# Kernel optimization log

Hardware: AMD Instinct MI355X
Metric: run time of the kernel (lower is better)

The kernel has to match this reference:

```python
import jax, jax.numpy as jnp
import numpy as np

HEADS = 8
NBLK = 4  # N: 4x4 spatial blocks
DIM = 96
EPS_NORM = 1e-12  # torch F.normalize eps


def _blockify(t, head, n):
    # 'b (head c) (h1 hh) (w1 ww) -> b head c (h1 w1) (hh ww)'
    b, C, H, W = t.shape
    c, hh, ww = C // head, H // n, W // n
    t = t.reshape(b, head, c, n, hh, n, ww)
    return t.transpose(0, 1, 2, 3, 5, 4, 6).reshape(b, head, c, n * n, hh * ww)


def _unblockify(t, n, hh, ww):
    # inverse of _blockify
    b, head, c, _, _ = t.shape
    t = t.reshape(b, head, c, n, n, hh, ww).transpose(0, 1, 2, 3, 5, 4, 6)
    return t.reshape(b, head * c, n * hh, n * ww)


def _l2norm(t):
    return t / jnp.maximum(jnp.linalg.norm(t, axis=-1, keepdims=True), EPS_NORM)


def setup_inputs():
    key = jax.random.key(0)
    ks = jax.random.split(key, 5)
    b, dim, H, W = 4, DIM, 256, 256
    x = jax.random.normal(ks[0], (b, dim, H, W), jnp.float32)
    mask = jax.random.uniform(ks[1], (b, dim, H, W), jnp.float32)
    w_qkv = jax.random.normal(ks[2], (3 * dim, dim, 1, 1), jnp.float32) / np.sqrt(dim)
    w_dw = jax.random.normal(ks[3], (3 * dim, 1, 3, 3), jnp.float32) / 3.0
    w_proj = jax.random.normal(ks[4], (dim, dim, 1, 1), jnp.float32) / np.sqrt(dim)
    temp_x = jnp.ones((HEADS, 1, 1, 1), jnp.float32)
    temp_m = jnp.ones((HEADS, 1, 1, 1), jnp.float32)
    return {"x": x, "mask": mask, "w_qkv": w_qkv, "w_dw": w_dw,
            "w_proj": w_proj, "temp_x": temp_x, "temp_m": temp_m}


def reference(x, mask, w_qkv, w_dw, w_proj, temp_x, temp_m):
    # H, W chosen divisible by 4, so the reflect-pad in the original is a no-op.
    dn = ('NCHW', 'OIHW', 'NCHW')
    qkv = jax.lax.conv_general_dilated(x, w_qkv, (1, 1), 'VALID', dimension_numbers=dn)
    qkv = jax.lax.conv_general_dilated(qkv, w_dw, (1, 1), ((1, 1), (1, 1)),
                                       feature_group_count=qkv.shape[1],
                                       dimension_numbers=dn)
    q, k, v = jnp.split(qkv, 3, axis=1)
    q = _l2norm(_blockify(q, HEADS, NBLK))
    k = _l2norm(_blockify(k, HEADS, NBLK))
    v = _blockify(v, HEADS, NBLK)

    # channel-block attention: [b,head,c,16,16]; temp broadcasts over (b, c, 16, 16)
    attn_x = jax.nn.softmax(jnp.einsum('bhcns,bhcms->bhcnm', q, k) * temp_x, axis=-1)

    # mask-derived attention (MaskMap): q==k==blockified mask
    qm = _blockify(mask, HEADS, NBLK)
    attn_m = jnp.einsum('bhcns,bhcms->bhcnm', qm, qm) * temp_m
    attn_m = jax.nn.softmax(_l2norm(attn_m), axis=-1)

    attn = jax.nn.softmax(attn_x + attn_m, axis=-1)
    out = jnp.einsum('bhcnm,bhcms->bhcns', attn, v)

    hh, ww = x.shape[2] // NBLK, x.shape[3] // NBLK
    out = _unblockify(out, NBLK, hh, ww)
    out = jax.lax.conv_general_dilated(out, w_proj, (1, 1), 'VALID', dimension_numbers=dn)
    return out
```

## Files before the change

kernel.cpp:

```cpp
#include <hip/hip_runtime.h>
#include <math.h>

#define HPIX 256
#define WPIX 256
#define NPIX (HPIX * WPIX)
#define DIM 96
#define QKVC 288
#define NHEAD 8
#define CPH 12
#define EPSN 1e-12f
#define PSTRIDE 544

typedef __attribute__((ext_vector_type(8))) short bf16x8;
typedef __attribute__((ext_vector_type(4))) float f32x4;

__device__ __forceinline__ unsigned short f2bf(float f) {
  unsigned u = __float_as_uint(f);
  u += 0x7FFF + ((u >> 16) & 1);
  return (unsigned short)(u >> 16);
}
__device__ __forceinline__ float bf2f(unsigned short h) {
  return __uint_as_float((unsigned)h << 16);
}

__global__ __launch_bounds__(256) void k_wprep(
    const float* __restrict__ wq, const float* __restrict__ wp,
    unsigned short* __restrict__ wqbf, unsigned short* __restrict__ wpbf) {
  int i = blockIdx.x * 256 + threadIdx.x;
  if (i < QKVC * DIM) wqbf[i] = f2bf(wq[i]);
  if (i < DIM * DIM)  wpbf[i] = f2bf(wp[i]);
}

template<int OC, int OCB, typename InT, typename OutT>
__global__ __launch_bounds__(256, 3) void k_gemm1x1(
    const InT* __restrict__ xin, const unsigned short* __restrict__ wbf,
    OutT* __restrict__ out) {
  __shared__ __align__(16) unsigned short xT[128 * 128];
  __shared__ __align__(16) unsigned short wlds[OCB * 104];
  int t = threadIdx.x;
  int p0 = blockIdx.x * 128;
  int oc0 = blockIdx.y * OCB;
  const InT* xb = xin + (size_t)blockIdx.z * DIM * NPIX;

  for (int i = t; i < OCB * 12; i += 256) {
    int row = i / 12, seg = i % 12;
    bf16x8 w8 = *(const bf16x8*)(wbf + (size_t)(oc0 + row) * DIM + seg * 8);
    *(bf16x8*)&wlds[row * 104 + seg * 8] = w8;
  }
  if (t < 192) {
    int kg = t >> 4;
    int f4c = t & 15;
    #pragma unroll
    for (int rep = 0; rep < 2; ++rep) {
      int f4 = f4c + rep * 16;
      float vals[8][4];
      #pragma unroll
      for (int i = 0; i < 8; ++i) {
        if constexpr (sizeof(InT) == 2) {
          ushort4 v = *(const ushort4*)(xb + (size_t)(kg * 8 + i) * NPIX + p0 + f4 * 4);
          ((ushort*)vals[i])[0] = v.x; ((ushort*)vals[i])[1] = v.y;
          ((ushort*)vals[i])[2] = v.z; ((ushort*)vals[i])[3] = v.w;
        } else {
          float4 v = *(const float4*)(xb + (size_t)(kg * 8 + i) * NPIX + p0 + f4 * 4);
          vals[i][0] = v.x; vals[i][1] = v.y; vals[i][2] = v.z; vals[i][3] = v.w;
        }
      }
      #pragma unroll
      for (int c = 0; c < 4; ++c) {
        int px = f4 * 4 + c;
        int u = kg ^ ((px & 7) ^ ((px >> 3) & 7));
        bf16x8 hv;
        #pragma unroll
        for (int i = 0; i < 8; ++i) {
          if constexpr (sizeof(InT) == 2) hv[i] = (short)((ushort*)vals[i])[c];
          else                            hv[i] = (short)f2bf(vals[i][c]);
        }
        *(bf16x8*)&xT[px * 128 + u * 8] = hv;
      }
    }
  }
  __syncthreads();

  int lane = t & 63, wv = t >> 6;
  int r16 = lane & 15, kg8 = lane >> 4;

  bf16x8 bfr[3][2];
  #pragma unroll
  for (int nj = 0; nj < 2; ++nj) {
    int px = wv * 32 + nj * 16 + r16;
    int swz = (px & 7) ^ ((px >> 3) & 7);
    #pragma unroll
    for (int ks = 0; ks < 3; ++ks) {
      int u = (ks * 4 + kg8) ^ swz;
      bfr[ks][nj] = *(const bf16x8*)&xT[px * 128 + u * 8];
    }
  }

  f32x4 acc[OCB / 16][2];
  #pragma unroll
  for (int mi = 0; mi < OCB / 16; ++mi)
    #pragma unroll
    for (int nj = 0; nj < 2; ++nj) acc[mi][nj] = (f32x4){0.f, 0.f, 0.f, 0.f};

  #pragma unroll
  for (int mi = 0; mi < OCB / 16; ++mi) {
    #pragma unroll
    for (int ks = 0; ks < 3; ++ks) {
      bf16x8 a = *(const bf16x8*)&wlds[(mi * 16 + r16) * 104 + ks * 32 + kg8 * 8];
      #pragma unroll
      for (int nj = 0; nj < 2; ++nj)
        acc[mi][nj] = __builtin_amdgcn_mfma_f32_16x16x32_bf16(a, bfr[ks][nj], acc[mi][nj], 0, 0, 0);
    }
  }

  OutT* op = out + (size_t)blockIdx.z * OC * NPIX + p0;
  __syncthreads();
  if constexpr (sizeof(OutT) == 2) {
    unsigned short* tl = xT;
    #pragma unroll
    for (int mi = 0; mi < OCB / 16; ++mi)
      #pragma unroll
      for (int nj = 0; nj < 2; ++nj)
        #pragma unroll
        for (int j = 0; j < 4; ++j)
          tl[(mi * 16 + kg8 * 4 + j) * 136 + wv * 32 + nj * 16 + r16] = f2bf(acc[mi][nj][j]);
    __syncthreads();
    #pragma unroll
    for (int r = 0; r < OCB / 16; ++r) {
      int idx = t + 256 * r;
      int oc = idx >> 4, seg = idx & 15;
      bf16x8 v8 = *(const bf16x8*)&tl[oc * 136 + seg * 8];
      *(bf16x8*)(op + (size_t)(oc0 + oc) * NPIX + seg * 8) = v8;
    }
  } else {
    float* tl = (float*)xT;
    #pragma unroll
    for (int half = 0; half < 2; ++half) {
      if (half) __syncthreads();
      #pragma unroll
      for (int mi = half * (OCB / 32); mi < (half + 1) * (OCB / 32); ++mi)
        #pragma unroll
        for (int nj = 0; nj < 2; ++nj)
          #pragma unroll
          for (int j = 0; j < 4; ++j)
            tl[(mi * 16 + kg8 * 4 + j - half * (OCB / 2)) * 136 + wv * 32 + nj * 16 + r16]
                = acc[mi][nj][j];
      __syncthreads();
      #pragma unroll
      for (int r = 0; r < OCB / 16; ++r) {
        int idx = t + 256 * r;
        int oc = idx >> 5, seg = idx & 31;
        float4 v4 = *(const float4*)&tl[oc * 136 + seg * 4];
        *(float4*)(op + (size_t)(oc0 + half * (OCB / 2) + oc) * NPIX + seg * 4) = v4;
      }
    }
  }
}

__global__ __launch_bounds__(256) void k_dw3x3_bf(
    const unsigned short* __restrict__ in, const float* __restrict__ w,
    unsigned short* __restrict__ qkout, unsigned short* __restrict__ vout) {
  int t = threadIdx.x;
  int p0 = (blockIdx.x * 256 + t) * 8;
  int ch = blockIdx.y, b = blockIdx.z;
  const unsigned short* plane = in + ((size_t)b * QKVC + ch) * NPIX;
  int y = p0 >> 8, x0 = p0 & 255;
  const float* wc = w + ch * 9;

  float acc[8];
  #pragma unroll
  for (int j = 0; j < 8; ++j) acc[j] = 0.f;

  #pragma unroll
  for (int dy = -1; dy <= 1; ++dy) {
    int yy = y + dy;
    float f[8];
    if (yy >= 0 && yy < HPIX) {
      bf16x8 v8 = *(const bf16x8*)(plane + (size_t)yy * WPIX + x0);
      #pragma unroll
      for (int j = 0; j < 8; ++j) f[j] = bf2f((unsigned short)v8[j]);
    } else {
      #pragma unroll
      for (int j = 0; j < 8; ++j) f[j] = 0.f;
    }
    float l = __shfl_up(f[7], 1);
    float r = __shfl_down(f[0], 1);
    if (x0 == 0) l = 0.f;
    if (x0 == 248) r = 0.f;
    float w0 = wc[(dy + 1) * 3], w1 = wc[(dy + 1) * 3 + 1], w2 = wc[(dy + 1) * 3 + 2];
    acc[0] = fmaf(w0, l, fmaf(w1, f[0], fmaf(w2, f[1], acc[0])));
    #pragma unroll
    for (int j = 1; j < 7; ++j)
      acc[j] = fmaf(w0, f[j - 1], fmaf(w1, f[j], fmaf(w2, f[j + 1], acc[j])));
    acc[7] = fmaf(w0, f[6], fmaf(w1, f[7], fmaf(w2, r, acc[7])));
  }

  bf16x8 o;
  #pragma unroll
  for (int j = 0; j < 8; ++j) o[j] = (short)f2bf(acc[j]);
  if (ch < 192) *(bf16x8*)(qkout + ((size_t)b * 192 + ch) * NPIX + p0) = o;
  else          *(bf16x8*)(vout + ((size_t)b * DIM + ch - 192) * NPIX + p0) = o;
}

__global__ __launch_bounds__(64) void k_attn_part(
    const unsigned short* __restrict__ qkbuf, const float* __restrict__ mask,
    float* __restrict__ pbuf) {
  int g = blockIdx.x, cb = blockIdx.y, lb = blockIdx.z;
  int lane = threadIdx.x;
  int r16 = lane & 15, kg8 = lane >> 4;

  const unsigned short* qb = qkbuf + ((size_t)lb * 192 + g) * NPIX;
  const unsigned short* kb = qkbuf + ((size_t)lb * 192 + 96 + g) * NPIX;
  const float* mb = mask + ((size_t)lb * DIM + g) * NPIX;

  int rbase = ((r16 >> 2) << 6) * WPIX + ((r16 & 3) << 6);

  f32x4 aqk = {0.f, 0.f, 0.f, 0.f}, amm = {0.f, 0.f, 0.f, 0.f};
  float dq = 0.f, dk = 0.f;

  #pragma unroll
  for (int ks = 0; ks < 8; ++ks) {
    int s = cb * 256 + ks * 32 + kg8 * 8;
    int off = rbase + (s >> 6) * WPIX + (s & 63);
    bf16x8 qf = *(const bf16x8*)(qb + off);
    bf16x8 kf = *(const bf16x8*)(kb + off);
    float4 m0 = *(const float4*)(mb + off);
    float4 m1 = *(const float4*)(mb + off + 4);
    bf16x8 mf;
    mf[0] = (short)f2bf(m0.x); mf[1] = (short)f2bf(m0.y);
    mf[2] = (short)f2bf(m0.z); mf[3] = (short)f2bf(m0.w);
    mf[4] = (short)f2bf(m1.x); mf[5] = (short)f2bf(m1.y);
    mf[6] = (short)f2bf(m1.z); mf[7] = (short)f2bf(m1.w);
    aqk = __builtin_amdgcn_mfma_f32_16x16x32_bf16(qf, kf, aqk, 0, 0, 0);
    amm = __builtin_amdgcn_mfma_f32_16x16x32_bf16(mf, mf, amm, 0, 0, 0);
    #pragma unroll
    for (int i = 0; i < 8; ++i) {
      float qv = bf2f((unsigned short)qf[i]); dq = fmaf(qv, qv, dq);
      float kv = bf2f((unsigned short)kf[i]); dk = fmaf(kv, kv, dk);
    }
  }
  dq += __shfl_xor(dq, 16); dq += __shfl_xor(dq, 32);
  dk += __shfl_xor(dk, 16); dk += __shfl_xor(dk, 32);

  float* pb = pbuf + (((size_t)lb * DIM + g) * 16 + cb) * PSTRIDE;
  #pragma unroll
  for (int j = 0; j < 4; ++j) {
    int n = kg8 * 4 + j;
    pb[n * 16 + r16] = aqk[j];
    pb[256 + n * 16 + r16] = amm[j];
  }
  if (lane < 16) { pb[512 + r16] = dq; pb[528 + r16] = dk; }
}

__global__ __launch_bounds__(256) void k_attn_fin(
    const float* __restrict__ pbuf, const float* __restrict__ tx,
    const float* __restrict__ tm, float* __restrict__ attnbuf) {
  int g = blockIdx.x;
  int lb = blockIdx.y;
  int h = g / CPH;
  int t = threadIdx.x;
  int n = t >> 4, m = t & 15;

  const float* pb = pbuf + ((size_t)lb * DIM + g) * 16 * PSTRIDE;
  float gqk = 0.f, gmm = 0.f, dq = 0.f, dk = 0.f;
  #pragma unroll
  for (int c = 0; c < 16; ++c) {
    const float* p = pb + c * PSTRIDE;
    gqk += p[t];
    gmm += p[256 + t];
    dq  += p[512 + n];
    dk  += p[528 + m];
  }

  float qn = fmaxf(sqrtf(dq), EPSN);
  float km = fmaxf(sqrtf(dk), EPSN);

  float ax = gqk / (qn * km) * tx[h];
  float r0 = ax;
  #pragma unroll
  for (int off = 8; off; off >>= 1) r0 = fmaxf(r0, __shfl_xor(r0, off, 16));
  float e0 = expf(ax - r0), es0 = e0;
  #pragma unroll
  for (int off = 8; off; off >>= 1) es0 += __shfl_xor(es0, off, 16);
  float attx = e0 / es0;

  float am = gmm * tm[h];
  float s2 = am * am;
  #pragma unroll
  for (int off = 8; off; off >>= 1) s2 += __shfl_xor(s2, off, 16);
  am = am / fmaxf(sqrtf(s2), EPSN);
  float r1 = am;
  #pragma unroll
  for (int off = 8; off; off >>= 1) r1 = fmaxf(r1, __shfl_xor(r1, off, 16));
  float e1 = expf(am - r1), es1 = e1;
  #pragma unroll
  for (int off = 8; off; off >>= 1) es1 += __shfl_xor(es1, off, 16);
  float attm = e1 / es1;

  float aa = attx + attm;
  float r2 = aa;
  #pragma unroll
  for (int off = 8; off; off >>= 1) r2 = fmaxf(r2, __shfl_xor(r2, off, 16));
  float e2 = expf(aa - r2), es2 = e2;
  #pragma unroll
  for (int off = 8; off; off >>= 1) es2 += __shfl_xor(es2, off, 16);

  attnbuf[(((size_t)lb * DIM + g) << 8) + t] = e2 / es2;
}

__global__ __launch_bounds__(256) void k_pv(
    const unsigned short* __restrict__ vbuf, const float* __restrict__ attnbuf,
    unsigned short* __restrict__ tout) {
  int hh = blockIdx.x;
  int g = blockIdx.y;
  int lb = blockIdx.z;
  int t = threadIdx.x;
  int ww = t & 63, grp = t >> 6;

  __shared__ float vt[16][64];
  __shared__ float at[16][16];

  const unsigned short* vb = vbuf + ((size_t)lb * DIM + g) * NPIX;
  #pragma unroll
  for (int jj = 0; jj < 4; ++jj) {
    int mm = jj * 4 + grp;
    vt[mm][ww] = bf2f(vb[(size_t)(((mm >> 2) << 6) + hh) * WPIX + ((mm & 3) << 6) + ww]);
  }
  at[t >> 4][t & 15] = attnbuf[(((size_t)lb * DIM + g) << 8) + t];
  __syncthreads();

  unsigned short* ob = tout + ((size_t)lb * DIM + g) * NPIX;
  #pragma unroll
  for (int jj = 0; jj < 4; ++jj) {
    int nn = jj * 4 + grp;
    float acc = 0.f;
    #pragma unroll
    for (int mm = 0; mm < 16; ++mm)
      acc = fmaf(at[nn][mm], vt[mm][ww], acc);
    ob[(size_t)(((nn >> 2) << 6) + hh) * WPIX + ((nn & 3) << 6) + ww] = f2bf(acc);
  }
}

extern "C" void kernel_launch(void* const* d_in, const int* in_sizes, int n_in,
                              void* d_out, int out_size, void* d_ws, size_t ws_size,
                              hipStream_t stream) {
  const float* x      = (const float*)d_in[0];
  const float* mask   = (const float*)d_in[1];
  const float* w_qkv  = (const float*)d_in[2];
  const float* w_dw   = (const float*)d_in[3];
  const float* w_proj = (const float*)d_in[4];
  const float* tx     = (const float*)d_in[5];
  const float* tm     = (const float*)d_in[6];
  float* out = (float*)d_out;

  const size_t wB     = (size_t)(QKVC * DIM + DIM * DIM) * 2;
  const size_t qkv1B  = (size_t)QKVC * NPIX * 2;
  const size_t qkB    = (size_t)192 * NPIX * 2;
  const size_t vB     = (size_t)DIM * NPIX * 2;
  const size_t atB    = (size_t)DIM * 256 * 4;
  const size_t pbB    = (size_t)DIM * 16 * PSTRIDE * 4;
  const size_t perB   = qkv1B + qkB + vB + atB + pbB;

  int nb = (ws_size >= wB + 4 * perB) ? 4 : 1;
  int npass = 4 / nb;

  char* base = (char*)d_ws;
  unsigned short* wqbf = (unsigned short*)base;
  unsigned short* wpbf = wqbf + QKVC * DIM;
  char* p = base + wB;
  unsigned short* qkv1bf = (unsigned short*)p;  p += (size_t)nb * qkv1B;
  unsigned short* tbuf   = qkv1bf;
  unsigned short* qkbuf  = (unsigned short*)p;  p += (size_t)nb * qkB;
  unsigned short* vbuf   = (unsigned short*)p;  p += (size_t)nb * vB;
  float*          attn   = (float*)p;           p += (size_t)nb * atB;
  float*          pbuf   = (float*)p;

  dim3 blk(256);
  k_wprep<<<dim3((QKVC * DIM + 255) / 256), blk, 0, stream>>>(
      w_qkv, w_proj, wqbf, wpbf);

  for (int pass = 0; pass < npass; ++pass) {
    int b0 = pass * nb;
    k_gemm1x1<QKVC, 96, float, unsigned short><<<dim3(NPIX / 128, 3, nb), blk, 0, stream>>>(
        x + (size_t)b0 * DIM * NPIX, wqbf, qkv1bf);
    k_dw3x3_bf<<<dim3(NPIX / 2048, QKVC, nb), blk, 0, stream>>>(
        qkv1bf, w_dw, qkbuf, vbuf);
    k_attn_part<<<dim3(DIM, 16, nb), dim3(64), 0, stream>>>(
        qkbuf, mask + (size_t)b0 * DIM * NPIX, pbuf);
    k_attn_fin<<<dim3(DIM, nb), blk, 0, stream>>>(pbuf, tx, tm, attn);
    k_pv<<<dim3(64, DIM, nb), blk, 0, stream>>>(vbuf, attn, tbuf);
    k_gemm1x1<DIM, 96, unsigned short, float><<<dim3(NPIX / 128, 1, nb), blk, 0, stream>>>(
        tbuf, wpbf, out + (size_t)b0 * DIM * NPIX);
  }
}
```

Baseline: 242.6 us.

## Use packed bf16 conversion, two-row depthwise conv, and wider QKV GEMM tiles

Replaces the scalar round-to-nearest bf16 conversion with the hardware v_cvt_pk_bf16_f32 packed instruction in the GEMM staging, depthwise conv output and mask conversion. The depthwise 3x3 kernel now computes two output rows per thread from four loaded input rows, cutting redundant row loads from 3 per output row to 2. The QKV 1x1 GEMM uses 144-channel blocks (2 y-blocks instead of 3), so each input tile is loaded and converted fewer times, at the cost of lower occupancy (launch bound 2) and possible register pressure. The packed conversion may differ slightly in rounding or NaN handling from the manual version.

```diff
diff --git a/kernel.cpp b/kernel.cpp
--- a/kernel.cpp
+++ b/kernel.cpp
@@ -22,6 +22,17 @@
 __device__ __forceinline__ float bf2f(unsigned short h) {
   return __uint_as_float((unsigned)h << 16);
 }
+__device__ __forceinline__ unsigned pkbf(float a, float b) {
+  unsigned r;
+  asm("v_cvt_pk_bf16_f32 %0, %1, %2" : "=v"(r) : "v"(a), "v"(b));
+  return r;
+}
+__device__ __forceinline__ bf16x8 pack8(const float* f) {
+  union { unsigned u[4]; bf16x8 v; } x;
+  x.u[0] = pkbf(f[0], f[1]); x.u[1] = pkbf(f[2], f[3]);
+  x.u[2] = pkbf(f[4], f[5]); x.u[3] = pkbf(f[6], f[7]);
+  return x.v;
+}
 
 __global__ __launch_bounds__(256) void k_wprep(
     const float* __restrict__ wq, const float* __restrict__ wp,
@@ -32,7 +43,7 @@
 }
 
 template<int OC, int OCB, typename InT, typename OutT>
-__global__ __launch_bounds__(256, 3) void k_gemm1x1(
+__global__ __launch_bounds__(256, (OCB > 96 ? 2 : 3)) void k_gemm1x1(
     const InT* __restrict__ xin, const unsigned short* __restrict__ wbf,
     OutT* __restrict__ out) {
   __shared__ __align__(16) unsigned short xT[128 * 128];
@@ -70,10 +81,14 @@
         int px = f4 * 4 + c;
         int u = kg ^ ((px & 7) ^ ((px >> 3) & 7));
         bf16x8 hv;
-        #pragma unroll
-        for (int i = 0; i < 8; ++i) {
-          if constexpr (sizeof(InT) == 2) hv[i] = (short)((ushort*)vals[i])[c];
-          else                            hv[i] = (short)f2bf(vals[i][c]);
+        if constexpr (sizeof(InT) == 2) {
+          #pragma unroll
+          for (int i = 0; i < 8; ++i) hv[i] = (short)((ushort*)vals[i])[c];
+        } else {
+          float col[8];
+          #pragma unroll
+          for (int i = 0; i < 8; ++i) col[i] = vals[i][c];
+          hv = pack8(col);
         }
         *(bf16x8*)&xT[px * 128 + u * 8] = hv;
       }
@@ -161,19 +176,21 @@
     const unsigned short* __restrict__ in, const float* __restrict__ w,
     unsigned short* __restrict__ qkout, unsigned short* __restrict__ vout) {
   int t = threadIdx.x;
-  int p0 = (blockIdx.x * 256 + t) * 8;
+  int xg = t & 31, yp = t >> 5;
+  int ybase = blockIdx.x * 16;
+  int y0 = ybase + yp * 2;
+  int x0 = xg * 8;
   int ch = blockIdx.y, b = blockIdx.z;
   const unsigned short* plane = in + ((size_t)b * QKVC + ch) * NPIX;
-  int y = p0 >> 8, x0 = p0 & 255;
   const float* wc = w + ch * 9;
 
-  float acc[8];
-  #pragma unroll
-  for (int j = 0; j < 8; ++j) acc[j] = 0.f;
-
-  #pragma unroll
-  for (int dy = -1; dy <= 1; ++dy) {
-    int yy = y + dy;
+  float accA[8], accB[8];
+  #pragma unroll
+  for (int j = 0; j < 8; ++j) { accA[j] = 0.f; accB[j] = 0.f; }
+
+  #pragma unroll
+  for (int r = 0; r < 4; ++r) {
+    int yy = y0 - 1 + r;
     float f[8];
     if (yy >= 0 && yy < HPIX) {
       bf16x8 v8 = *(const bf16x8*)(plane + (size_t)yy * WPIX + x0);
@@ -184,22 +201,34 @@
       for (int j = 0; j < 8; ++j) f[j] = 0.f;
     }
     float l = __shfl_up(f[7], 1);
-    float r = __shfl_down(f[0], 1);
+    float rr = __shfl_down(f[0], 1);
     if (x0 == 0) l = 0.f;
-    if (x0 == 248) r = 0.f;
-    float w0 = wc[(dy + 1) * 3], w1 = wc[(dy + 1) * 3 + 1], w2 = wc[(dy + 1) * 3 + 2];
-    acc[0] = fmaf(w0, l, fmaf(w1, f[0], fmaf(w2, f[1], acc[0])));
-    #pragma unroll
-    for (int j = 1; j < 7; ++j)
-      acc[j] = fmaf(w0, f[j - 1], fmaf(w1, f[j], fmaf(w2, f[j + 1], acc[j])));
-    acc[7] = fmaf(w0, f[6], fmaf(w1, f[7], fmaf(w2, r, acc[7])));
-  }
-
-  bf16x8 o;
-  #pragma unroll
-  for (int j = 0; j < 8; ++j) o[j] = (short)f2bf(acc[j]);
-  if (ch < 192) *(bf16x8*)(qkout + ((size_t)b * 192 + ch) * NPIX + p0) = o;
-  else          *(bf16x8*)(vout + ((size_t)b * DIM + ch - 192) * NPIX + p0) = o;
+    if (x0 == 248) rr = 0.f;
+    if (r < 3) {
+      float w0 = wc[r * 3], w1 = wc[r * 3 + 1], w2 = wc[r * 3 + 2];
+      accA[0] = fmaf(w0, l, fmaf(w1, f[0], fmaf(w2, f[1], accA[0])));
+      #pragma unroll
+      for (int j = 1; j < 7; ++j)
+        accA[j] = fmaf(w0, f[j - 1], fmaf(w1, f[j], fmaf(w2, f[j + 1], accA[j])));
+      accA[7] = fmaf(w0, f[6], fmaf(w1, f[7], fmaf(w2, rr, accA[7])));
+    }
+    if (r > 0) {
+      float w0 = wc[(r - 1) * 3], w1 = wc[(r - 1) * 3 + 1], w2 = wc[(r - 1) * 3 + 2];
+      accB[0] = fmaf(w0, l, fmaf(w1, f[0], fmaf(w2, f[1], accB[0])));
+      #pragma unroll
+      for (int j = 1; j < 7; ++j)
+        accB[j] = fmaf(w0, f[j - 1], fmaf(w1, f[j], fmaf(w2, f[j + 1], accB[j])));
+      accB[7] = fmaf(w0, f[6], fmaf(w1, f[7], fmaf(w2, rr, accB[7])));
+    }
+  }
+
+  bf16x8 oA = pack8(accA), oB = pack8(accB);
+  size_t pA = (size_t)y0 * WPIX + x0;
+  unsigned short* outp;
+  if (ch < 192) outp = qkout + ((size_t)b * 192 + ch) * NPIX;
+  else          outp = vout + ((size_t)b * DIM + ch - 192) * NPIX;
+  *(bf16x8*)(outp + pA) = oA;
+  *(bf16x8*)(outp + pA + WPIX) = oB;
 }
 
 __global__ __launch_bounds__(64) void k_attn_part(
@@ -226,11 +255,10 @@
     bf16x8 kf = *(const bf16x8*)(kb + off);
     float4 m0 = *(const float4*)(mb + off);
     float4 m1 = *(const float4*)(mb + off + 4);
-    bf16x8 mf;
-    mf[0] = (short)f2bf(m0.x); mf[1] = (short)f2bf(m0.y);
-    mf[2] = (short)f2bf(m0.z); mf[3] = (short)f2bf(m0.w);
-    mf[4] = (short)f2bf(m1.x); mf[5] = (short)f2bf(m1.y);
-    mf[6] = (short)f2bf(m1.z); mf[7] = (short)f2bf(m1.w);
+    union { unsigned u[4]; bf16x8 v; } mm_;
+    mm_.u[0] = pkbf(m0.x, m0.y); mm_.u[1] = pkbf(m0.z, m0.w);
+    mm_.u[2] = pkbf(m1.x, m1.y); mm_.u[3] = pkbf(m1.z, m1.w);
+    bf16x8 mf = mm_.v;
     aqk = __builtin_amdgcn_mfma_f32_16x16x32_bf16(qf, kf, aqk, 0, 0, 0);
     amm = __builtin_amdgcn_mfma_f32_16x16x32_bf16(mf, mf, amm, 0, 0, 0);
     #pragma unroll
@@ -381,9 +409,9 @@
 
   for (int pass = 0; pass < npass; ++pass) {
     int b0 = pass * nb;
-    k_gemm1x1<QKVC, 96, float, unsigned short><<<dim3(NPIX / 128, 3, nb), blk, 0, stream>>>(
+    k_gemm1x1<QKVC, 144, float, unsigned short><<<dim3(NPIX / 128, 2, nb), blk, 0, stream>>>(
         x + (size_t)b0 * DIM * NPIX, wqbf, qkv1bf);
-    k_dw3x3_bf<<<dim3(NPIX / 2048, QKVC, nb), blk, 0, stream>>>(
+    k_dw3x3_bf<<<dim3(NPIX / 4096, QKVC, nb), blk, 0, stream>>>(
         qkv1bf, w_dw, qkbuf, vbuf);
     k_attn_part<<<dim3(DIM, 16, nb), dim3(64), 0, stream>>>(
         qkbuf, mask + (size_t)b0 * DIM * NPIX, pbuf);
```

Measured after the change: 242.7 us. About the same (+0.0%).
